# Performance work log

Hardware: AMD Instinct MI355X
Metric: run time of the kernel (lower is better)

Reference implementation:

```python
import jax, jax.numpy as jnp
import numpy as np

H = 512      # hidden_size
F = 1024     # expert_hidden_size
E = 16       # expert_count
EPS = 1e-5   # torch LayerNorm default eps


def setup_inputs() -> dict:
    key = jax.random.key(0)
    ks = jax.random.split(key, 7)
    tokens = jax.random.normal(ks[0], (4, 2048, H), dtype=jnp.float32)
    # Stacked per-expert parameters (one 3D tensor per parameter kind)
    ln_g = jnp.ones((E, H), dtype=jnp.float32)
    ln_b = jnp.zeros((E, H), dtype=jnp.float32)
    W1 = jax.random.normal(ks[1], (E, H, F), dtype=jnp.float32) * (1.0 / np.sqrt(H))
    b1 = jax.random.normal(ks[2], (E, F), dtype=jnp.float32) * 0.01
    W2 = jax.random.normal(ks[3], (E, F, H), dtype=jnp.float32) * (1.0 / np.sqrt(F))
    b2 = jax.random.normal(ks[4], (E, H), dtype=jnp.float32) * 0.01
    return {"tokens": tokens, "ln_g": ln_g, "ln_b": ln_b,
            "W1": W1, "b1": b1, "W2": W2, "b2": b2}


def reference(tokens, ln_g, ln_b, W1, b1, W2, b2):
    # LayerNorm statistics depend only on tokens, so compute x_hat once
    mu = jnp.mean(tokens, axis=-1, keepdims=True)
    var = jnp.mean(jnp.square(tokens - mu), axis=-1, keepdims=True)
    x_hat = (tokens - mu) * jax.lax.rsqrt(var + EPS)          # [B,S,H]
    # Per-expert affine: [B,S,E,H]
    xin = x_hat[:, :, None, :] * ln_g + ln_b
    h = jnp.einsum('bseh,ehf->bsef', xin, W1) + b1            # [B,S,E,F]
    h = jax.nn.gelu(h, approximate=False)                     # torch GELU default (erf)
    out = jnp.einsum('bsef,efh->bseh', h, W2) + b2            # [B,S,E,H] (stack dim=2)
    return out
```

## Files before the change

### kernel.cpp

```cpp
#include <hip/hip_runtime.h>
#include <stdint.h>

#define H 512
#define F 1024
#define E 16
#define TOK 8192
#define EPS 1e-5f

typedef short bf16x8 __attribute__((ext_vector_type(8)));
typedef float f32x4 __attribute__((ext_vector_type(4)));

__device__ __forceinline__ float bf2f(unsigned short u) {
    union { unsigned int i; float f; } v; v.i = ((unsigned int)u) << 16; return v.f;
}
__device__ __forceinline__ unsigned short f2bf(float f) {
    union { float f; unsigned int i; } v; v.f = f;
    unsigned int r = (v.i + 0x7FFFu + ((v.i >> 16) & 1u)) >> 16;
    return (unsigned short)r;
}
__device__ __forceinline__ void gload16(const void* g, void* l) {
    __builtin_amdgcn_global_load_lds(
        (const __attribute__((address_space(1))) unsigned int*)g,
        (__attribute__((address_space(3))) unsigned int*)l, 16, 0, 0);
}

__device__ __forceinline__ float gelu_erf(float v) {
    const float x  = v * 0.70710678118654752f;
    const float ax = fabsf(x);
    const float t  = __builtin_amdgcn_rcpf(fmaf(0.3275911f, ax, 1.0f));
    float p = fmaf(1.061405429f, t, -1.453152027f);
    p = fmaf(p, t, 1.421413741f);
    p = fmaf(p, t, -0.284496736f);
    p = fmaf(p, t, 0.254829592f);
    p = p * t;
    const float ex = __expf(-x * x);
    float er = fmaf(-p, ex, 1.0f);
    er = copysignf(er, x);
    return 0.5f * v * (1.0f + er);
}

__global__ void ln_kernel(const float* __restrict__ tokens,
                          unsigned short* __restrict__ xhat) {
    const int tid  = threadIdx.x;
    const int wid  = tid >> 6;
    const int lane = tid & 63;
    const int token = blockIdx.x * 4 + wid;

    const float* src = tokens + (size_t)token * H + lane * 8;
    float4 r0 = *reinterpret_cast<const float4*>(src);
    float4 r1 = *reinterpret_cast<const float4*>(src + 4);
    float x[8] = {r0.x, r0.y, r0.z, r0.w, r1.x, r1.y, r1.z, r1.w};

    float s = 0.f, s2 = 0.f;
#pragma unroll
    for (int j = 0; j < 8; ++j) { s += x[j]; s2 += x[j] * x[j]; }
#pragma unroll
    for (int m = 32; m >= 1; m >>= 1) {
        s  += __shfl_xor(s, m);
        s2 += __shfl_xor(s2, m);
    }
    const float mu  = s * (1.0f / H);
    float var = s2 * (1.0f / H) - mu * mu;
    var = fmaxf(var, 0.0f);
    const float rstd = rsqrtf(var + EPS);

    unsigned short o[8];
#pragma unroll
    for (int j = 0; j < 8; ++j) o[j] = f2bf((x[j] - mu) * rstd);
    uint4 w;
    w.x = o[0] | ((unsigned)o[1] << 16);
    w.y = o[2] | ((unsigned)o[3] << 16);
    w.z = o[4] | ((unsigned)o[5] << 16);
    w.w = o[6] | ((unsigned)o[7] << 16);
    *reinterpret_cast<uint4*>(xhat + (size_t)token * H + lane * 8) = w;
}

#define XPAD 72
__global__ void transpose_kernel(const float* __restrict__ src,
                                 unsigned short* __restrict__ dst,
                                 int rows, int cols,
                                 const float* __restrict__ scale) {
    __shared__ __align__(16) unsigned short tile[64 * XPAD];
    const int e  = blockIdx.z;
    const int r0 = blockIdx.y * 64;
    const int c0 = blockIdx.x * 64;
    const int tid = threadIdx.x;

    const float* sbase = src + (size_t)e * rows * cols;
    unsigned short* dbase = dst + (size_t)e * rows * cols;

    {
        const int r  = tid >> 2;
        const int cg = (tid & 3) * 16;
        const float* p = sbase + (size_t)(r0 + r) * cols + c0 + cg;
        const float sc = (scale != nullptr) ? scale[e * rows + r0 + r] : 1.0f;
        unsigned short u[16];
#pragma unroll
        for (int j = 0; j < 16; j += 4) {
            float4 v = *reinterpret_cast<const float4*>(p + j);
            u[j + 0] = f2bf(v.x * sc);
            u[j + 1] = f2bf(v.y * sc);
            u[j + 2] = f2bf(v.z * sc);
            u[j + 3] = f2bf(v.w * sc);
        }
#pragma unroll
        for (int j = 0; j < 16; j += 8) {
            uint4 w;
            w.x = u[j + 0] | ((unsigned)u[j + 1] << 16);
            w.y = u[j + 2] | ((unsigned)u[j + 3] << 16);
            w.z = u[j + 4] | ((unsigned)u[j + 5] << 16);
            w.w = u[j + 6] | ((unsigned)u[j + 7] << 16);
            *reinterpret_cast<uint4*>(&tile[r * XPAD + cg + j]) = w;
        }
    }
    __syncthreads();
#pragma unroll
    for (int i = 0; i < 2; ++i) {
        const int oc = (tid >> 3) + i * 32;
        const int og = (tid & 7) * 8;
        unsigned short u[8];
#pragma unroll
        for (int j = 0; j < 8; ++j) u[j] = tile[(og + j) * XPAD + oc];
        uint4 w;
        w.x = u[0] | ((unsigned)u[1] << 16);
        w.y = u[2] | ((unsigned)u[3] << 16);
        w.z = u[4] | ((unsigned)u[5] << 16);
        w.w = u[6] | ((unsigned)u[7] << 16);
        *reinterpret_cast<uint4*>(dbase + (size_t)(c0 + oc) * rows + r0 + og) = w;
    }
}

__global__ void b1fold_kernel(const float* __restrict__ b1,
                              const float* __restrict__ lnb,
                              const float* __restrict__ W1,
                              float* __restrict__ b1p) {
    __shared__ float slb[64];
    const int e = blockIdx.y;
    const int z = blockIdx.z;
    const int f = blockIdx.x * 256 + threadIdx.x;
    const int h0 = z * 64;
    if (threadIdx.x < 64) slb[threadIdx.x] = lnb[e * H + h0 + threadIdx.x];
    __syncthreads();
    float acc = (z == 0) ? b1[e * F + f] : 0.0f;
    const float* w = W1 + (size_t)e * H * F + (size_t)h0 * F + f;
#pragma unroll 8
    for (int h = 0; h < 64; ++h) acc += slb[h] * w[(size_t)h * F];
    atomicAdd(&b1p[e * F + f], acc);
}

__global__ __launch_bounds__(256, 3) void gemm1_kernel(
    const unsigned short* __restrict__ xhat,
    const unsigned short* __restrict__ w1gt,
    const float* __restrict__ b1p,
    unsigned short* __restrict__ hbuf)
{
    __shared__ __align__(16) unsigned short lds_x[128 * 64];
    __shared__ __align__(16) unsigned short lds_w[128 * 64];

    const int tid  = threadIdx.x;
    const int lane = tid & 63;
    const int wid  = tid >> 6;
    const int quad = lane >> 4;
    const int l16  = lane & 15;

    const unsigned bid = blockIdx.x;
    const int e  = bid & 15;
    const int t  = bid >> 4;
    const int ft = t & 7;
    const int mt = t >> 3;
    const int m0 = mt * 128, f0 = ft * 128;
    const int wm = wid & 1, wn = wid >> 1;

    f32x4 acc[4][4];
#pragma unroll
    for (int mi = 0; mi < 4; ++mi)
#pragma unroll
        for (int ni = 0; ni < 4; ++ni) acc[mi][ni] = (f32x4){0.f, 0.f, 0.f, 0.f};

    const unsigned short* xg = xhat + (size_t)m0 * H;
    const unsigned short* wg = w1gt + ((size_t)e * F + f0) * H;
    const int swzr = (l16 & 7) * 8;

    for (int kt = 0; kt < 8; ++kt) {
        const int k0 = kt * 64;
        __syncthreads();
#pragma unroll
        for (int i = 0; i < 4; ++i) {
            const int idx = tid + i * 256;
            const int row = idx >> 3;
            const int c   = ((idx & 7) * 8) ^ ((row & 7) * 8);
            gload16(xg + (size_t)row * H + k0 + c, (char*)lds_x + (size_t)idx * 16);
            gload16(wg + (size_t)row * H + k0 + c, (char*)lds_w + (size_t)idx * 16);
        }
        __syncthreads();
#pragma unroll
        for (int ks = 0; ks < 2; ++ks) {
            const int kc = (ks * 32 + quad * 8) ^ swzr;
            bf16x8 a[4], b[4];
#pragma unroll
            for (int i = 0; i < 4; ++i)
                a[i] = *reinterpret_cast<const bf16x8*>(&lds_x[(wm * 64 + i * 16 + l16) * 64 + kc]);
#pragma unroll
            for (int i = 0; i < 4; ++i)
                b[i] = *reinterpret_cast<const bf16x8*>(&lds_w[(wn * 64 + i * 16 + l16) * 64 + kc]);
#pragma unroll
            for (int mi = 0; mi < 4; ++mi)
#pragma unroll
                for (int ni = 0; ni < 4; ++ni)
                    acc[mi][ni] = __builtin_amdgcn_mfma_f32_16x16x32_bf16(a[mi], b[ni], acc[mi][ni], 0, 0, 0);
        }
    }

    float bv[4];
#pragma unroll
    for (int ni = 0; ni < 4; ++ni)
        bv[ni] = b1p[e * F + f0 + wn * 64 + ni * 16 + l16];
#pragma unroll
    for (int mi = 0; mi < 4; ++mi) {
#pragma unroll
        for (int r = 0; r < 4; ++r) {
            const int row = m0 + wm * 64 + mi * 16 + quad * 4 + r;
            unsigned short* dst = hbuf + ((size_t)row * E + e) * F + f0;
#pragma unroll
            for (int ni = 0; ni < 4; ++ni) {
                const float v = acc[mi][ni][r] + bv[ni];
                dst[wn * 64 + ni * 16 + l16] = f2bf(gelu_erf(v));
            }
        }
    }
}

__global__ __launch_bounds__(512, 4) void gemm2_kernel(
    const unsigned short* __restrict__ hbuf,
    const unsigned short* __restrict__ w2t,
    const float* __restrict__ b2,
    float* __restrict__ outp)
{
    __shared__ __align__(16) unsigned short lds_a[64 * 64];
    __shared__ __align__(16) unsigned short lds_b[512 * 64];

    const int tid  = threadIdx.x;
    const int lane = tid & 63;
    const int w    = tid >> 6;
    const int quad = lane >> 4;
    const int l16  = lane & 15;
    const int swzr = (l16 & 7) * 8;

    const int e  = blockIdx.x & 15;
    const int mt = blockIdx.x >> 4;
    const int m0 = mt * 64;

    f32x4 acc[4][4];
#pragma unroll
    for (int mi = 0; mi < 4; ++mi)
#pragma unroll
        for (int ni = 0; ni < 4; ++ni) acc[mi][ni] = (f32x4){0.f, 0.f, 0.f, 0.f};

    const unsigned short* hg = hbuf + ((size_t)m0 * E + e) * F;
    const unsigned short* wg = w2t + (size_t)e * H * F;

    const int ar = tid >> 3;
    const int ac = ((tid & 7) * 8) ^ ((ar & 7) * 8);

    for (int kt = 0; kt < 16; ++kt) {
        const int k0 = kt * 64;
        __syncthreads();
        gload16(hg + (size_t)ar * (E * F) + k0 + ac, (char*)lds_a + (size_t)tid * 16);
#pragma unroll
        for (int i = 0; i < 8; ++i) {
            const int idx = tid + i * 512;
            const int row = idx >> 3;
            const int c   = ((idx & 7) * 8) ^ ((row & 7) * 8);
            gload16(wg + (size_t)row * F + k0 + c, (char*)lds_b + (size_t)idx * 16);
        }
        __syncthreads();
#pragma unroll
        for (int ks = 0; ks < 2; ++ks) {
            const int kcb = ks * 32 + quad * 8;
            const int kc  = kcb ^ swzr;
            bf16x8 a[4], b[4];
#pragma unroll
            for (int i = 0; i < 4; ++i)
                a[i] = *reinterpret_cast<const bf16x8*>(&lds_a[(i * 16 + l16) * 64 + kc]);
#pragma unroll
            for (int ni = 0; ni < 4; ++ni)
                b[ni] = *reinterpret_cast<const bf16x8*>(&lds_b[(w * 64 + ni * 16 + l16) * 64 + kc]);
#pragma unroll
            for (int ni = 0; ni < 4; ++ni)
#pragma unroll
                for (int mi = 0; mi < 4; ++mi)
                    acc[mi][ni] = __builtin_amdgcn_mfma_f32_16x16x32_bf16(a[mi], b[ni], acc[mi][ni], 0, 0, 0);
        }
    }

    float bv[4];
#pragma unroll
    for (int ni = 0; ni < 4; ++ni)
        bv[ni] = b2[e * H + w * 64 + ni * 16 + l16];
#pragma unroll
    for (int mi = 0; mi < 4; ++mi) {
#pragma unroll
        for (int r = 0; r < 4; ++r) {
            const int row = m0 + mi * 16 + quad * 4 + r;
            float* dst = outp + ((size_t)row * E + e) * H + w * 64;
#pragma unroll
            for (int ni = 0; ni < 4; ++ni)
                dst[ni * 16 + l16] = acc[mi][ni][r] + bv[ni];
        }
    }
}

extern "C" void kernel_launch(void* const* d_in, const int* in_sizes, int n_in,
                              void* d_out, int out_size, void* d_ws, size_t ws_size,
                              hipStream_t stream) {
    const float* tokens = (const float*)d_in[0];
    const float* ln_g   = (const float*)d_in[1];
    const float* ln_b   = (const float*)d_in[2];
    const float* W1     = (const float*)d_in[3];
    const float* b1     = (const float*)d_in[4];
    const float* W2     = (const float*)d_in[5];
    const float* b2     = (const float*)d_in[6];

    char* ws = (char*)d_ws;
    unsigned short* xhat = (unsigned short*)(ws);
    unsigned short* w1gt = (unsigned short*)(ws + 8388608);
    unsigned short* w2t  = (unsigned short*)(ws + 25165824);
    float*          b1p  = (float*)(ws + 41943040);

    unsigned short* hbuf = (unsigned short*)d_out;
    float*          outp = (float*)d_out;

    hipMemsetAsync(b1p, 0, E * F * sizeof(float), stream);
    hipLaunchKernelGGL(ln_kernel, dim3(TOK / 4), dim3(256), 0, stream, tokens, xhat);
    hipLaunchKernelGGL(transpose_kernel, dim3(F / 64, H / 64, E), dim3(256), 0, stream,
                       W1, w1gt, H, F, ln_g);
    hipLaunchKernelGGL(transpose_kernel, dim3(H / 64, F / 64, E), dim3(256), 0, stream,
                       W2, w2t, F, H, (const float*)nullptr);
    hipLaunchKernelGGL(b1fold_kernel, dim3(F / 256, E, 8), dim3(256), 0, stream, b1, ln_b, W1, b1p);
    hipLaunchKernelGGL(gemm1_kernel, dim3(E * (TOK / 128) * (F / 128)), dim3(256), 0, stream,
                       xhat, w1gt, b1p, hbuf);
    hipLaunchKernelGGL(gemm2_kernel, dim3(E * (TOK / 64)), dim3(512), 0, stream,
                       hbuf, w2t, b2, outp);
}
```

Before: 717.1 us.

## Double-buffer LDS and enlarge block tiles in both expert GEMMs

Both GEMM kernels now use 1024-thread blocks with larger M tiles (256 rows for gemm1, 128 for gemm2). They also double-buffer their LDS tiles, so the next K-slice is fetched with global_load_lds while MFMAs run on the current one. This is meant to hide global-load latency behind compute and cut the barrier pairs per K step to one. In exchange, LDS per block grows a lot (about 96KB and 160KB), which likely limits each CU to one block. gemm1 also shrinks each wave's tile to 32x64, lowering register reuse per wave.

```diff
diff --git a/kernel.cpp b/kernel.cpp
--- a/kernel.cpp
+++ b/kernel.cpp
@@ -148,96 +148,14 @@
     atomicAdd(&b1p[e * F + f], acc);
 }
 
-__global__ __launch_bounds__(256, 3) void gemm1_kernel(
+__global__ __launch_bounds__(1024, 4) void gemm1_kernel(
     const unsigned short* __restrict__ xhat,
     const unsigned short* __restrict__ w1gt,
     const float* __restrict__ b1p,
     unsigned short* __restrict__ hbuf)
 {
-    __shared__ __align__(16) unsigned short lds_x[128 * 64];
-    __shared__ __align__(16) unsigned short lds_w[128 * 64];
-
-    const int tid  = threadIdx.x;
-    const int lane = tid & 63;
-    const int wid  = tid >> 6;
-    const int quad = lane >> 4;
-    const int l16  = lane & 15;
-
-    const unsigned bid = blockIdx.x;
-    const int e  = bid & 15;
-    const int t  = bid >> 4;
-    const int ft = t & 7;
-    const int mt = t >> 3;
-    const int m0 = mt * 128, f0 = ft * 128;
-    const int wm = wid & 1, wn = wid >> 1;
-
-    f32x4 acc[4][4];
-#pragma unroll
-    for (int mi = 0; mi < 4; ++mi)
-#pragma unroll
-        for (int ni = 0; ni < 4; ++ni) acc[mi][ni] = (f32x4){0.f, 0.f, 0.f, 0.f};
-
-    const unsigned short* xg = xhat + (size_t)m0 * H;
-    const unsigned short* wg = w1gt + ((size_t)e * F + f0) * H;
-    const int swzr = (l16 & 7) * 8;
-
-    for (int kt = 0; kt < 8; ++kt) {
-        const int k0 = kt * 64;
-        __syncthreads();
-#pragma unroll
-        for (int i = 0; i < 4; ++i) {
-            const int idx = tid + i * 256;
-            const int row = idx >> 3;
-            const int c   = ((idx & 7) * 8) ^ ((row & 7) * 8);
-            gload16(xg + (size_t)row * H + k0 + c, (char*)lds_x + (size_t)idx * 16);
-            gload16(wg + (size_t)row * H + k0 + c, (char*)lds_w + (size_t)idx * 16);
-        }
-        __syncthreads();
-#pragma unroll
-        for (int ks = 0; ks < 2; ++ks) {
-            const int kc = (ks * 32 + quad * 8) ^ swzr;
-            bf16x8 a[4], b[4];
-#pragma unroll
-            for (int i = 0; i < 4; ++i)
-                a[i] = *reinterpret_cast<const bf16x8*>(&lds_x[(wm * 64 + i * 16 + l16) * 64 + kc]);
-#pragma unroll
-            for (int i = 0; i < 4; ++i)
-                b[i] = *reinterpret_cast<const bf16x8*>(&lds_w[(wn * 64 + i * 16 + l16) * 64 + kc]);
-#pragma unroll
-            for (int mi = 0; mi < 4; ++mi)
-#pragma unroll
-                for (int ni = 0; ni < 4; ++ni)
-                    acc[mi][ni] = __builtin_amdgcn_mfma_f32_16x16x32_bf16(a[mi], b[ni], acc[mi][ni], 0, 0, 0);
-        }
-    }
-
-    float bv[4];
-#pragma unroll
-    for (int ni = 0; ni < 4; ++ni)
-        bv[ni] = b1p[e * F + f0 + wn * 64 + ni * 16 + l16];
-#pragma unroll
-    for (int mi = 0; mi < 4; ++mi) {
-#pragma unroll
-        for (int r = 0; r < 4; ++r) {
-            const int row = m0 + wm * 64 + mi * 16 + quad * 4 + r;
-            unsigned short* dst = hbuf + ((size_t)row * E + e) * F + f0;
-#pragma unroll
-            for (int ni = 0; ni < 4; ++ni) {
-                const float v = acc[mi][ni][r] + bv[ni];
-                dst[wn * 64 + ni * 16 + l16] = f2bf(gelu_erf(v));
-            }
-        }
-    }
-}
-
-__global__ __launch_bounds__(512, 4) void gemm2_kernel(
-    const unsigned short* __restrict__ hbuf,
-    const unsigned short* __restrict__ w2t,
-    const float* __restrict__ b2,
-    float* __restrict__ outp)
-{
-    __shared__ __align__(16) unsigned short lds_a[64 * 64];
-    __shared__ __align__(16) unsigned short lds_b[512 * 64];
+    __shared__ __align__(16) unsigned short lds_x[2 * 256 * 64];
+    __shared__ __align__(16) unsigned short lds_w[2 * 128 * 64];
 
     const int tid  = threadIdx.x;
     const int lane = tid & 63;
@@ -246,9 +164,106 @@
     const int l16  = lane & 15;
     const int swzr = (l16 & 7) * 8;
 
+    const unsigned bid = blockIdx.x;
+    const int e  = bid & 15;
+    const int t  = bid >> 4;
+    const int ft = t & 7;
+    const int mt = t >> 3;
+    const int m0 = mt * 256, f0 = ft * 128;
+    const int wm = w >> 1, wn = w & 1;
+
+    f32x4 acc[2][4];
+#pragma unroll
+    for (int mi = 0; mi < 2; ++mi)
+#pragma unroll
+        for (int ni = 0; ni < 4; ++ni) acc[mi][ni] = (f32x4){0.f, 0.f, 0.f, 0.f};
+
+    const unsigned short* xg = xhat + (size_t)m0 * H;
+    const unsigned short* wg = w1gt + ((size_t)e * F + f0) * H;
+
+    auto stage = [&](int kt, int buf) {
+        const int k0 = kt * 64;
+#pragma unroll
+        for (int i = 0; i < 2; ++i) {
+            const int idx = tid + i * 1024;
+            const int row = idx >> 3;
+            const int c   = ((idx & 7) * 8) ^ ((row & 7) * 8);
+            gload16(xg + (size_t)row * H + k0 + c,
+                    (char*)lds_x + (size_t)buf * 32768 + (size_t)idx * 16);
+        }
+        {
+            const int row = tid >> 3;
+            const int c   = ((tid & 7) * 8) ^ ((row & 7) * 8);
+            gload16(wg + (size_t)row * H + k0 + c,
+                    (char*)lds_w + (size_t)buf * 16384 + (size_t)tid * 16);
+        }
+    };
+
+    stage(0, 0);
+    __syncthreads();
+    for (int kt = 0; kt < 8; ++kt) {
+        const int cur = kt & 1;
+        if (kt < 7) stage(kt + 1, cur ^ 1);
+#pragma unroll
+        for (int ks = 0; ks < 2; ++ks) {
+            const int kc = (ks * 32 + quad * 8) ^ swzr;
+            bf16x8 a[2], b[4];
+#pragma unroll
+            for (int mi = 0; mi < 2; ++mi)
+                a[mi] = *reinterpret_cast<const bf16x8*>(
+                    &lds_x[cur * 16384 + (wm * 32 + mi * 16 + l16) * 64 + kc]);
+#pragma unroll
+            for (int ni = 0; ni < 4; ++ni)
+                b[ni] = *reinterpret_cast<const bf16x8*>(
+                    &lds_w[cur * 8192 + (wn * 64 + ni * 16 + l16) * 64 + kc]);
+#pragma unroll
+            for (int mi = 0; mi < 2; ++mi)
+#pragma unroll
+                for (int ni = 0; ni < 4; ++ni)
+                    acc[mi][ni] = __builtin_amdgcn_mfma_f32_16x16x32_bf16(a[mi], b[ni], acc[mi][ni], 0, 0, 0);
+        }
+        __syncthreads();
+    }
+
+    float bv[4];
+#pragma unroll
+    for (int ni = 0; ni < 4; ++ni)
+        bv[ni] = b1p[e * F + f0 + wn * 64 + ni * 16 + l16];
+#pragma unroll
+    for (int mi = 0; mi < 2; ++mi) {
+#pragma unroll
+        for (int r = 0; r < 4; ++r) {
+            const int row = m0 + wm * 32 + mi * 16 + quad * 4 + r;
+            unsigned short* dst = hbuf + ((size_t)row * E + e) * F + f0;
+#pragma unroll
+            for (int ni = 0; ni < 4; ++ni) {
+                const float v = acc[mi][ni][r] + bv[ni];
+                dst[wn * 64 + ni * 16 + l16] = f2bf(gelu_erf(v));
+            }
+        }
+    }
+}
+
+__global__ __launch_bounds__(1024, 4) void gemm2_kernel(
+    const unsigned short* __restrict__ hbuf,
+    const unsigned short* __restrict__ w2t,
+    const float* __restrict__ b2,
+    float* __restrict__ outp)
+{
+    __shared__ __align__(16) unsigned short lds_a[2 * 128 * 64];
+    __shared__ __align__(16) unsigned short lds_b[2 * 512 * 64];
+
+    const int tid  = threadIdx.x;
+    const int lane = tid & 63;
+    const int w    = tid >> 6;
+    const int quad = lane >> 4;
+    const int l16  = lane & 15;
+    const int swzr = (l16 & 7) * 8;
+
     const int e  = blockIdx.x & 15;
     const int mt = blockIdx.x >> 4;
-    const int m0 = mt * 64;
+    const int m0 = mt * 128;
+    const int wm = w & 1, wn = w >> 1;
 
     f32x4 acc[4][4];
 #pragma unroll
@@ -259,50 +274,60 @@
     const unsigned short* hg = hbuf + ((size_t)m0 * E + e) * F;
     const unsigned short* wg = w2t + (size_t)e * H * F;
 
-    const int ar = tid >> 3;
-    const int ac = ((tid & 7) * 8) ^ ((ar & 7) * 8);
-
-    for (int kt = 0; kt < 16; ++kt) {
+    auto stage = [&](int kt, int buf) {
         const int k0 = kt * 64;
-        __syncthreads();
-        gload16(hg + (size_t)ar * (E * F) + k0 + ac, (char*)lds_a + (size_t)tid * 16);
-#pragma unroll
-        for (int i = 0; i < 8; ++i) {
-            const int idx = tid + i * 512;
+        {
+            const int row = tid >> 3;
+            const int c   = ((tid & 7) * 8) ^ ((row & 7) * 8);
+            gload16(hg + (size_t)row * (E * F) + k0 + c,
+                    (char*)lds_a + (size_t)buf * 16384 + (size_t)tid * 16);
+        }
+#pragma unroll
+        for (int i = 0; i < 4; ++i) {
+            const int idx = tid + i * 1024;
             const int row = idx >> 3;
             const int c   = ((idx & 7) * 8) ^ ((row & 7) * 8);
-            gload16(wg + (size_t)row * F + k0 + c, (char*)lds_b + (size_t)idx * 16);
-        }
-        __syncthreads();
+            gload16(wg + (size_t)row * F + k0 + c,
+                    (char*)lds_b + (size_t)buf * 65536 + (size_t)idx * 16);
+        }
+    };
+
+    stage(0, 0);
+    __syncthreads();
+    for (int kt = 0; kt < 16; ++kt) {
+        const int cur = kt & 1;
+        if (kt < 15) stage(kt + 1, cur ^ 1);
 #pragma unroll
         for (int ks = 0; ks < 2; ++ks) {
-            const int kcb = ks * 32 + quad * 8;
-            const int kc  = kcb ^ swzr;
+            const int kc = (ks * 32 + quad * 8) ^ swzr;
             bf16x8 a[4], b[4];
 #pragma unroll
-            for (int i = 0; i < 4; ++i)
-                a[i] = *reinterpret_cast<const bf16x8*>(&lds_a[(i * 16 + l16) * 64 + kc]);
+            for (int mi = 0; mi < 4; ++mi)
+                a[mi] = *reinterpret_cast<const bf16x8*>(
+                    &lds_a[cur * 8192 + (wm * 64 + mi * 16 + l16) * 64 + kc]);
 #pragma unroll
             for (int ni = 0; ni < 4; ++ni)
-                b[ni] = *reinterpret_cast<const bf16x8*>(&lds_b[(w * 64 + ni * 16 + l16) * 64 + kc]);
+                b[ni] = *reinterpret_cast<const bf16x8*>(
+                    &lds_b[cur * 32768 + (wn * 64 + ni * 16 + l16) * 64 + kc]);
 #pragma unroll
             for (int ni = 0; ni < 4; ++ni)
 #pragma unroll
                 for (int mi = 0; mi < 4; ++mi)
                     acc[mi][ni] = __builtin_amdgcn_mfma_f32_16x16x32_bf16(a[mi], b[ni], acc[mi][ni], 0, 0, 0);
         }
+        __syncthreads();
     }
 
     float bv[4];
 #pragma unroll
     for (int ni = 0; ni < 4; ++ni)
-        bv[ni] = b2[e * H + w * 64 + ni * 16 + l16];
+        bv[ni] = b2[e * H + wn * 64 + ni * 16 + l16];
 #pragma unroll
     for (int mi = 0; mi < 4; ++mi) {
 #pragma unroll
         for (int r = 0; r < 4; ++r) {
-            const int row = m0 + mi * 16 + quad * 4 + r;
-            float* dst = outp + ((size_t)row * E + e) * H + w * 64;
+            const int row = m0 + wm * 64 + mi * 16 + quad * 4 + r;
+            float* dst = outp + ((size_t)row * E + e) * H + wn * 64;
 #pragma unroll
             for (int ni = 0; ni < 4; ++ni)
                 dst[ni * 16 + l16] = acc[mi][ni][r] + bv[ni];
@@ -337,8 +362,8 @@
     hipLaunchKernelGGL(transpose_kernel, dim3(H / 64, F / 64, E), dim3(256), 0, stream,
                        W2, w2t, F, H, (const float*)nullptr);
     hipLaunchKernelGGL(b1fold_kernel, dim3(F / 256, E, 8), dim3(256), 0, stream, b1, ln_b, W1, b1p);
-    hipLaunchKernelGGL(gemm1_kernel, dim3(E * (TOK / 128) * (F / 128)), dim3(256), 0, stream,
+    hipLaunchKernelGGL(gemm1_kernel, dim3(E * (TOK / 256) * (F / 128)), dim3(1024), 0, stream,
                        xhat, w1gt, b1p, hbuf);
-    hipLaunchKernelGGL(gemm2_kernel, dim3(E * (TOK / 64)), dim3(512), 0, stream,
+    hipLaunchKernelGGL(gemm2_kernel, dim3(E * (TOK / 128)), dim3(1024), 0, stream,
                        hbuf, w2t, b2, outp);
 }
```

New measurement: 749.1 us. +4.5%, slower.
